# Kernel optimization log

Hardware: AMD Instinct MI355X
Metric: run time of the kernel (lower is better)

Reference implementation:

```python
import jax, jax.numpy as jnp
import numpy as np

DOWNSAMPLE = 4
OUT_RATIO = 8


def _avg_pool(x, k):
    b, c, h, w = x.shape
    return x.reshape(b, c, h // k, k, w // k, k).mean(axis=(3, 5))


def _upsample_axis(x, axis, scale):
    # bilinear, align_corners=True along one axis
    n = x.shape[axis]
    m = n * scale
    coords = jnp.arange(m, dtype=x.dtype) * ((n - 1) / (m - 1))
    i0 = jnp.floor(coords).astype(jnp.int32)
    i1 = jnp.minimum(i0 + 1, n - 1)
    f = coords - i0.astype(x.dtype)
    x0 = jnp.take(x, i0, axis=axis)
    x1 = jnp.take(x, i1, axis=axis)
    shp = [1] * x.ndim
    shp[axis] = m
    f = f.reshape(shp)
    return x0 * (1 - f) + x1 * f


def _upsample_bilinear(x, scale):
    return _upsample_axis(_upsample_axis(x, 2, scale), 3, scale)


def _conv1x1(x, W, b):
    # x: (b,c,h,w), W: (out,in), b: (out,)
    return jnp.einsum('bchw,oc->bohw', x, W) + b[None, :, None, None]


def setup_inputs() -> dict:
    key = jax.random.key(0)
    ks = jax.random.split(key, 8)
    C = 64
    Cq = C // OUT_RATIO
    s = 1.0 / np.sqrt(C)
    x = jax.random.normal(ks[0], (8, C, 256, 256), dtype=jnp.float32)
    Wq = jax.random.uniform(ks[1], (Cq, C), jnp.float32, -s, s)
    bq = jax.random.uniform(ks[2], (Cq,), jnp.float32, -s, s)
    Wk = jax.random.uniform(ks[3], (Cq, C), jnp.float32, -s, s)
    bk = jax.random.uniform(ks[4], (Cq,), jnp.float32, -s, s)
    Wv = jax.random.uniform(ks[5], (C, C), jnp.float32, -s, s)
    bv = jax.random.uniform(ks[6], (C,), jnp.float32, -s, s)
    gamma = jax.random.normal(ks[7], (1,), jnp.float32) * 0.1
    return {"x": x, "Wq": Wq, "bq": bq, "Wk": Wk, "bk": bk, "Wv": Wv, "bv": bv, "gamma": gamma}


def reference(x, Wq, bq, Wk, bk, Wv, bv, gamma):
    b, c, h, w = x.shape
    xd = _avg_pool(x, DOWNSAMPLE)          # (b, c, hd, wd)
    hd, wd = xd.shape[2], xd.shape[3]
    n = hd * wd
    q = _conv1x1(xd, Wq, bq).reshape(b, -1, n)   # (b, cq, n)
    k = _conv1x1(xd, Wk, bk).reshape(b, -1, n)   # (b, cq, n)
    v = _conv1x1(xd, Wv, bv).reshape(b, c, n)    # (b, c, n)
    energy = jnp.einsum('bci,bcj->bij', q, k)    # (b, n, n), no scaling (as in source)
    attn = jax.nn.softmax(energy, axis=-1)
    out = jnp.einsum('bcj,bij->bci', v, attn)    # out[b,c,i] = sum_j v[b,c,j]*attn[b,i,j]
    out = out.reshape(b, c, hd, wd)
    out = _upsample_bilinear(out, DOWNSAMPLE)    # back to (b, c, h, w)
    return gamma[0] * out + x
```

## Files before the change

kernel.cpp:

```cpp
#include <hip/hip_runtime.h>
#include <hip/hip_bf16.h>

#define CCH 64
#define NPIX 4096

typedef __attribute__((ext_vector_type(8))) short short8;
typedef __attribute__((ext_vector_type(16))) float f32x16;

union U4S8 { uint4 u; short8 s; };

__device__ inline uint32_t pk2bf(float lo, float hi) {
    __hip_bfloat162 h = __float22bfloat162_rn(make_float2(lo, hi));
    return *reinterpret_cast<uint32_t*>(&h);
}

__global__ __launch_bounds__(256, 2) void pool_conv_kernel(
    const float* __restrict__ x,
    const float* __restrict__ Wq, const float* __restrict__ bq,
    const float* __restrict__ Wk, const float* __restrict__ bk,
    const float* __restrict__ Wv, const float* __restrict__ bv,
    __hip_bfloat16* __restrict__ Qo, __hip_bfloat16* __restrict__ Ko,
    __hip_bfloat16* __restrict__ VPo)
{
    const int blk  = blockIdx.x;
    const int b    = blk >> 6;
    const int ptg  = blk & 63;
    const int t    = threadIdx.x;
    const int lane = t & 63;
    const int w    = t >> 6;
    const int l31  = lane & 31;
    const int hi   = lane >> 5;

    __shared__ __align__(16) __hip_bfloat16 xdt[64][72];
    __shared__ __align__(16) __hip_bfloat16 otile[80][72];
    __shared__ float sbias[96];

    if (t < 96) {
        float v = 0.f;
        if (t < 8)       v = bq[t];
        else if (t < 16) v = bk[t-8];
        else if (t < 80) v = bv[t-16];
        sbias[t] = v;
    }

    const float* xbase = x + (size_t)(b*CCH)*65536 + (size_t)(ptg*4)*256 + lane*4;
    #pragma unroll 4
    for (int cc = 0; cc < 16; ++cc) {
        const int c = w*16 + cc;
        const float* xp = xbase + (size_t)c*65536;
        float4 v0 = *(const float4*)(xp);
        float4 v1 = *(const float4*)(xp + 256);
        float4 v2 = *(const float4*)(xp + 512);
        float4 v3 = *(const float4*)(xp + 768);
        float s = (v0.x+v0.y+v0.z+v0.w) + (v1.x+v1.y+v1.z+v1.w)
                + (v2.x+v2.y+v2.z+v2.w) + (v3.x+v3.y+v3.z+v3.w);
        xdt[lane][c] = __float2bfloat16(s * 0.0625f);
    }

    const int  ptt  = w & 1;
    const int  octA = (w < 2) ? 0 : 2;
    const bool hasB = (w < 2);

    short8 wfA[4], wfB[4];
    auto loadW = [&](int oct, short8* wf) {
        const int row = oct*32 + l31;
        const float* wr = nullptr;
        if (row < 8)       wr = Wq + row*CCH;
        else if (row < 16) wr = Wk + (row-8)*CCH;
        else if (row < 80) wr = Wv + (row-16)*CCH;
        #pragma unroll
        for (int kt = 0; kt < 4; ++kt) {
            U4S8 f;
            if (wr) {
                const int c0 = kt*16 + hi*8;
                float4 a = *(const float4*)(wr + c0);
                float4 d = *(const float4*)(wr + c0 + 4);
                f.u.x = pk2bf(a.x, a.y); f.u.y = pk2bf(a.z, a.w);
                f.u.z = pk2bf(d.x, d.y); f.u.w = pk2bf(d.z, d.w);
            } else {
                f.u = make_uint4(0,0,0,0);
            }
            wf[kt] = f.s;
        }
    };
    loadW(octA, wfA);
    if (hasB) loadW(1, wfB);

    __syncthreads();

    short8 xf[4];
    #pragma unroll
    for (int kt = 0; kt < 4; ++kt)
        xf[kt] = *(const short8*)&xdt[ptt*32 + l31][kt*16 + hi*8];

    f32x16 accA, accB;
    #pragma unroll
    for (int r = 0; r < 16; ++r) { accA[r] = 0.f; accB[r] = 0.f; }
    #pragma unroll
    for (int kt = 0; kt < 4; ++kt)
        accA = __builtin_amdgcn_mfma_f32_32x32x16_bf16(wfA[kt], xf[kt], accA, 0, 0, 0);
    if (hasB) {
        #pragma unroll
        for (int kt = 0; kt < 4; ++kt)
            accB = __builtin_amdgcn_mfma_f32_32x32x16_bf16(wfB[kt], xf[kt], accB, 0, 0, 0);
    }

    {
        const int pt = ptt*32 + l31;
        #pragma unroll
        for (int r = 0; r < 16; ++r) {
            const int row = (r&3) + 8*(r>>2) + 4*hi;
            const int oc  = octA*32 + row;
            if (oc < 80) otile[oc][pt] = __float2bfloat16(accA[r] + sbias[oc]);
        }
        if (hasB) {
            #pragma unroll
            for (int r = 0; r < 16; ++r) {
                const int row = (r&3) + 8*(r>>2) + 4*hi;
                const int oc  = 32 + row;
                otile[oc][pt] = __float2bfloat16(accB[r] + sbias[oc]);
            }
        }
    }
    __syncthreads();

    if (t < 128) {
        const int p = t & 63;
        const int oc0 = (t < 64) ? 0 : 8;
        unsigned short v[8];
        #pragma unroll
        for (int j = 0; j < 8; ++j)
            v[j] = *reinterpret_cast<const unsigned short*>(&otile[oc0 + j][p]);
        uint4 q;
        q.x = (uint32_t)v[0] | ((uint32_t)v[1] << 16);
        q.y = (uint32_t)v[2] | ((uint32_t)v[3] << 16);
        q.z = (uint32_t)v[4] | ((uint32_t)v[5] << 16);
        q.w = (uint32_t)v[6] | ((uint32_t)v[7] << 16);
        __hip_bfloat16* dst = (t < 64) ? Qo : Ko;
        *(uint4*)(dst + ((size_t)b*NPIX + ptg*64 + p)*8) = q;
    }
    {
        __hip_bfloat16* vdst = VPo + ((size_t)b*512 + (size_t)ptg*8)*512;
        const int c31 = t & 31;
        const int h2  = (t >> 5) & 1;
        const int ct  = (t >> 6) & 1;
        const int s1  = (t >> 7) & 1;
        const int row = 16 + ct*32 + c31;
        const int pt0 = s1*16 + h2*8;
        uint4 u0 = *(const uint4*)&otile[row][pt0];
        uint4 u1 = *(const uint4*)&otile[row][pt0 + 32];
        *(uint4*)(vdst + t*8)        = u0;
        *(uint4*)(vdst + 2048 + t*8) = u1;
    }
}

__global__ __launch_bounds__(256, 4) void attn_kernel(
    const __hip_bfloat16* __restrict__ Q, const __hip_bfloat16* __restrict__ K,
    const __hip_bfloat16* __restrict__ VP, float* __restrict__ OS)
{
    const int bb   = blockIdx.x;
    const int b    = bb & 7;
    const int qg   = bb >> 3;
    const int i0   = qg * 32;
    const int t    = threadIdx.x;
    const int lane = t & 63;
    const int kvq  = t >> 6;
    const int l31  = lane & 31;
    const int hi   = lane >> 5;

    __shared__ float tiles[4][64][33];
    __shared__ float ml[4][2][32];
    __shared__ float fs[4][32];
    __shared__ float ils[32];

    U4S8 qf;
    if (hi == 0) qf.u = *(const uint4*)(Q + ((size_t)b*NPIX + i0 + l31)*8);
    else         qf.u = make_uint4(0,0,0,0);

    f32x16 acc0, acc1, zacc;
    #pragma unroll
    for (int r = 0; r < 16; ++r) { acc0[r] = 0.f; acc1[r] = 0.f; zacc[r] = 0.f; }
    float m = -1e30f, l = 0.f;

    const __hip_bfloat16* Kb  = K  + (size_t)b*NPIX*8;
    const __hip_bfloat16* VPb = VP + (size_t)b*512*512;

    auto ldK = [&](int kv) {
        U4S8 r;
        if (hi == 0) r.u = *(const uint4*)(Kb + (size_t)(kv + l31)*8);
        else         r.u = make_uint4(0,0,0,0);
        return r;
    };
    auto ldVP = [&](int chg, int s1, int ct) {
        U4S8 r;
        r.u = *(const uint4*)(VPb + ((size_t)((chg*2 + s1)*2 + ct))*512 + lane*8);
        return r;
    };

    int kv0 = kvq * 1024;
    U4S8 kf = ldK(kv0);
    U4S8 v00 = ldVP(kv0>>5, 0, 0), v10 = ldVP(kv0>>5, 0, 1);
    U4S8 v01 = ldVP(kv0>>5, 1, 0), v11 = ldVP(kv0>>5, 1, 1);

    #pragma unroll 1
    for (int ch = 0; ch < 32; ++ch) {
        U4S8 ckf = kf, cv00 = v00, cv01 = v01, cv10 = v10, cv11 = v11;
        const int nkv0 = kv0 + 32;
        kf  = ldK(nkv0);
        v00 = ldVP(nkv0>>5, 0, 0); v10 = ldVP(nkv0>>5, 0, 1);
        v01 = ldVP(nkv0>>5, 1, 0); v11 = ldVP(nkv0>>5, 1, 1);

        f32x16 s = __builtin_amdgcn_mfma_f32_32x32x16_bf16(ckf.s, qf.s, zacc, 0, 0, 0);

        float mx = fmaxf(s[0], s[1]);
        #pragma unroll
        for (int r = 2; r < 16; ++r) mx = fmaxf(mx, s[r]);
        mx = fmaxf(mx, __shfl_xor(mx, 32));

        if (!__all(mx <= m + 8.f)) {
            float mnew = fmaxf(m, mx);
            float sc = __expf(m - mnew);
            l *= sc; m = mnew;
            #pragma unroll
            for (int r = 0; r < 16; ++r) { acc0[r] *= sc; acc1[r] *= sc; }
        }

        float p[16];
        float ssum = 0.f;
        #pragma unroll
        for (int r = 0; r < 16; ++r) { p[r] = __expf(s[r] - m); ssum += p[r]; }
        ssum += __shfl_xor(ssum, 32);
        l += ssum;

        uint32_t W01 = pk2bf(p[0],  p[1]),  W23 = pk2bf(p[2],  p[3]);
        uint32_t W45 = pk2bf(p[4],  p[5]),  W67 = pk2bf(p[6],  p[7]);
        uint32_t W89 = pk2bf(p[8],  p[9]),  Wab = pk2bf(p[10], p[11]);
        uint32_t Wcd = pk2bf(p[12], p[13]), Wef = pk2bf(p[14], p[15]);
        uint32_t W45p = (uint32_t)__shfl_xor((int)W45, 32);
        uint32_t W67p = (uint32_t)__shfl_xor((int)W67, 32);
        uint32_t W01p = (uint32_t)__shfl_xor((int)W01, 32);
        uint32_t W23p = (uint32_t)__shfl_xor((int)W23, 32);
        uint32_t Wcdp = (uint32_t)__shfl_xor((int)Wcd, 32);
        uint32_t Wefp = (uint32_t)__shfl_xor((int)Wef, 32);
        uint32_t W89p = (uint32_t)__shfl_xor((int)W89, 32);
        uint32_t Wabp = (uint32_t)__shfl_xor((int)Wab, 32);
        U4S8 pb0, pb1;
        pb0.u.x = hi ? W45p : W01;   pb0.u.y = hi ? W67p : W23;
        pb0.u.z = hi ? W45  : W01p;  pb0.u.w = hi ? W67  : W23p;
        pb1.u.x = hi ? Wcdp : W89;   pb1.u.y = hi ? Wefp : Wab;
        pb1.u.z = hi ? Wcd  : W89p;  pb1.u.w = hi ? Wef  : Wabp;

        acc0 = __builtin_amdgcn_mfma_f32_32x32x16_bf16(cv00.s, pb0.s, acc0, 0, 0, 0);
        acc1 = __builtin_amdgcn_mfma_f32_32x32x16_bf16(cv10.s, pb0.s, acc1, 0, 0, 0);
        acc0 = __builtin_amdgcn_mfma_f32_32x32x16_bf16(cv01.s, pb1.s, acc0, 0, 0, 0);
        acc1 = __builtin_amdgcn_mfma_f32_32x32x16_bf16(cv11.s, pb1.s, acc1, 0, 0, 0);

        kv0 = nkv0;
    }

    #pragma unroll
    for (int r = 0; r < 16; ++r) {
        const int cr = (r&3) + 8*(r>>2) + 4*hi;
        tiles[kvq][cr]     [l31] = acc0[r];
        tiles[kvq][cr + 32][l31] = acc1[r];
    }
    if (hi == 0) { ml[kvq][0][l31] = m; ml[kvq][1][l31] = l; }
    __syncthreads();

    if (t < 32) {
        float m0 = ml[0][0][t], m1 = ml[1][0][t], m2 = ml[2][0][t], m3 = ml[3][0][t];
        float ms = fmaxf(fmaxf(m0, m1), fmaxf(m2, m3));
        float f0 = __expf(m0-ms), f1 = __expf(m1-ms), f2 = __expf(m2-ms), f3 = __expf(m3-ms);
        fs[0][t] = f0; fs[1][t] = f1; fs[2][t] = f2; fs[3][t] = f3;
        ils[t] = 1.f / (ml[0][1][t]*f0 + ml[1][1][t]*f1 + ml[2][1][t]*f2 + ml[3][1][t]*f3);
    }
    __syncthreads();

    float* outp = OS + (size_t)b*CCH*NPIX + i0;
    const int c  = t >> 2;
    const int q8 = (t & 3) * 8;
    float o[8];
    #pragma unroll
    for (int j = 0; j < 8; ++j) {
        const int q = q8 + j;
        float v = tiles[0][c][q]*fs[0][q] + tiles[1][c][q]*fs[1][q]
                + tiles[2][c][q]*fs[2][q] + tiles[3][c][q]*fs[3][q];
        o[j] = v * ils[q];
    }
    *(float4*)(outp + (size_t)c*NPIX + q8)     = make_float4(o[0], o[1], o[2], o[3]);
    *(float4*)(outp + (size_t)c*NPIX + q8 + 4) = make_float4(o[4], o[5], o[6], o[7]);
}

__global__ __launch_bounds__(256) void upsample_add_kernel(
    const float* __restrict__ OS, const float* __restrict__ x,
    const float* __restrict__ gamma, float* __restrict__ out)
{
    const size_t qidx = (size_t)blockIdx.x * 256 + threadIdx.x;
    const size_t idx  = qidx * 4;
    const float g = gamma[0];
    const int w4 = (int)(idx & 255);
    const int h  = (int)((idx >> 8) & 255);
    const size_t bc = idx >> 16;

    const float scale = 63.0f / 255.0f;
    float fh = h * scale; int h0 = (int)fh; float fy = fh - (float)h0; int h1 = min(h0+1, 63);

    const float* r0 = OS + bc * (size_t)NPIX + h0*64;
    const float* r1 = OS + bc * (size_t)NPIX + h1*64;
    float4 xi = *(const float4*)(x + idx);

    float o[4];
    #pragma unroll
    for (int j = 0; j < 4; ++j) {
        const int w = w4 + j;
        float fw = w * scale; int w0 = (int)fw; float fx = fw - (float)w0; int w1 = min(w0+1, 63);
        float a0 = r0[w0], a1 = r0[w1], b0 = r1[w0], b1 = r1[w1];
        float vt = a0 + (a1 - a0) * fx;
        float vb = b0 + (b1 - b0) * fx;
        o[j] = vt + (vb - vt) * fy;
    }
    float4 ov;
    ov.x = g*o[0] + xi.x; ov.y = g*o[1] + xi.y;
    ov.z = g*o[2] + xi.z; ov.w = g*o[3] + xi.w;
    *(float4*)(out + idx) = ov;
}

extern "C" void kernel_launch(void* const* d_in, const int* in_sizes, int n_in,
                              void* d_out, int out_size, void* d_ws, size_t ws_size,
                              hipStream_t stream) {
    const float* x     = (const float*)d_in[0];
    const float* Wq    = (const float*)d_in[1];
    const float* bq    = (const float*)d_in[2];
    const float* Wk    = (const float*)d_in[3];
    const float* bk    = (const float*)d_in[4];
    const float* Wv    = (const float*)d_in[5];
    const float* bv    = (const float*)d_in[6];
    const float* gamma = (const float*)d_in[7];
    float* out = (float*)d_out;

    char* ws = (char*)d_ws;
    __hip_bfloat16* Qb = (__hip_bfloat16*)(ws);
    __hip_bfloat16* Kb = (__hip_bfloat16*)(ws + (size_t)( 512<<10));
    __hip_bfloat16* VP = (__hip_bfloat16*)(ws + (size_t)(1024<<10));
    float*          OS = (float*)         (ws + (size_t)(5120<<10));

    pool_conv_kernel<<<512, 256, 0, stream>>>(x, Wq, bq, Wk, bk, Wv, bv, Qb, Kb, VP);
    attn_kernel<<<1024, 256, 0, stream>>>(Qb, Kb, VP, OS);
    const size_t total4 = (size_t)8 * 64 * 256 * 256 / 4;
    upsample_add_kernel<<<(int)(total4 / 256), 256, 0, stream>>>(OS, x, gamma, out);
}
```

Measured before the change: 118.6 us.

## Permute V layout at write so attention P operand needs no lane shuffles

The attention kernel previously rearranged the bf16-packed softmax probabilities across half-waves with eight shfl_xor operations per iteration to match the MFMA B-operand layout. The pool/conv kernel now writes the V tile in a permuted pixel order so the probabilities can be packed directly in register order, removing those cross-lane shuffles and selects from the inner loop. It also fully unrolls the channel pooling loop. The V reordering must line up exactly with the MFMA k-index mapping, and the V store now does four 8-byte LDS reads instead of two 16-byte ones.

```diff
diff --git a/kernel.cpp b/kernel.cpp
--- a/kernel.cpp
+++ b/kernel.cpp
@@ -44,7 +44,7 @@
     }
 
     const float* xbase = x + (size_t)(b*CCH)*65536 + (size_t)(ptg*4)*256 + lane*4;
-    #pragma unroll 4
+    #pragma unroll
     for (int cc = 0; cc < 16; ++cc) {
         const int c = w*16 + cc;
         const float* xp = xbase + (size_t)c*65536;
@@ -146,11 +146,13 @@
         const int ct  = (t >> 6) & 1;
         const int s1  = (t >> 7) & 1;
         const int row = 16 + ct*32 + c31;
-        const int pt0 = s1*16 + h2*8;
-        uint4 u0 = *(const uint4*)&otile[row][pt0];
-        uint4 u1 = *(const uint4*)&otile[row][pt0 + 32];
-        *(uint4*)(vdst + t*8)        = u0;
-        *(uint4*)(vdst + 2048 + t*8) = u1;
+        const int pt0 = s1*16 + h2*4;
+        uint2 a0 = *(const uint2*)&otile[row][pt0];
+        uint2 a1 = *(const uint2*)&otile[row][pt0 + 8];
+        uint2 b0 = *(const uint2*)&otile[row][pt0 + 32];
+        uint2 b1 = *(const uint2*)&otile[row][pt0 + 40];
+        *(uint4*)(vdst + t*8)        = make_uint4(a0.x, a0.y, a1.x, a1.y);
+        *(uint4*)(vdst + 2048 + t*8) = make_uint4(b0.x, b0.y, b1.x, b1.y);
     }
 }
 
@@ -232,23 +234,11 @@
         ssum += __shfl_xor(ssum, 32);
         l += ssum;
 
-        uint32_t W01 = pk2bf(p[0],  p[1]),  W23 = pk2bf(p[2],  p[3]);
-        uint32_t W45 = pk2bf(p[4],  p[5]),  W67 = pk2bf(p[6],  p[7]);
-        uint32_t W89 = pk2bf(p[8],  p[9]),  Wab = pk2bf(p[10], p[11]);
-        uint32_t Wcd = pk2bf(p[12], p[13]), Wef = pk2bf(p[14], p[15]);
-        uint32_t W45p = (uint32_t)__shfl_xor((int)W45, 32);
-        uint32_t W67p = (uint32_t)__shfl_xor((int)W67, 32);
-        uint32_t W01p = (uint32_t)__shfl_xor((int)W01, 32);
-        uint32_t W23p = (uint32_t)__shfl_xor((int)W23, 32);
-        uint32_t Wcdp = (uint32_t)__shfl_xor((int)Wcd, 32);
-        uint32_t Wefp = (uint32_t)__shfl_xor((int)Wef, 32);
-        uint32_t W89p = (uint32_t)__shfl_xor((int)W89, 32);
-        uint32_t Wabp = (uint32_t)__shfl_xor((int)Wab, 32);
         U4S8 pb0, pb1;
-        pb0.u.x = hi ? W45p : W01;   pb0.u.y = hi ? W67p : W23;
-        pb0.u.z = hi ? W45  : W01p;  pb0.u.w = hi ? W67  : W23p;
-        pb1.u.x = hi ? Wcdp : W89;   pb1.u.y = hi ? Wefp : Wab;
-        pb1.u.z = hi ? Wcd  : W89p;  pb1.u.w = hi ? Wef  : Wabp;
+        pb0.u.x = pk2bf(p[0],  p[1]);  pb0.u.y = pk2bf(p[2],  p[3]);
+        pb0.u.z = pk2bf(p[4],  p[5]);  pb0.u.w = pk2bf(p[6],  p[7]);
+        pb1.u.x = pk2bf(p[8],  p[9]);  pb1.u.y = pk2bf(p[10], p[11]);
+        pb1.u.z = pk2bf(p[12], p[13]); pb1.u.w = pk2bf(p[14], p[15]);
 
         acc0 = __builtin_amdgcn_mfma_f32_32x32x16_bf16(cv00.s, pb0.s, acc0, 0, 0, 0);
         acc1 = __builtin_amdgcn_mfma_f32_32x32x16_bf16(cv10.s, pb0.s, acc1, 0, 0, 0);
```

After: 115.1 us. 1.03x faster.
